# Kernel tuning notes

Measured on AMD Instinct MI355X. Metric: run time of the kernel, lower is better.

Reference implementation:

```python
import jax, jax.numpy as jnp
import numpy as np

HIDDEN = 3584
N_HEADS = 28
N_KV_HEADS = 4
HEAD_DIM = 128
ROPE_BASE = 10000.0
SCALE = HEAD_DIM ** -0.5
T = 2048


def setup_inputs() -> dict:
    key = jax.random.key(0)
    ks = jax.random.split(key, 8)
    s = HIDDEN ** -0.5
    return {
        "positions": jnp.arange(T, dtype=jnp.int64),
        "hidden_states": jax.random.normal(ks[0], (T, HIDDEN), dtype=jnp.float32),
        "wq": jax.random.normal(ks[1], (N_HEADS * HEAD_DIM, HIDDEN), dtype=jnp.float32) * s,
        "bq": jax.random.normal(ks[2], (N_HEADS * HEAD_DIM,), dtype=jnp.float32) * 0.02,
        "wk": jax.random.normal(ks[3], (N_KV_HEADS * HEAD_DIM, HIDDEN), dtype=jnp.float32) * s,
        "bk": jax.random.normal(ks[4], (N_KV_HEADS * HEAD_DIM,), dtype=jnp.float32) * 0.02,
        "wv": jax.random.normal(ks[5], (N_KV_HEADS * HEAD_DIM, HIDDEN), dtype=jnp.float32) * s,
        "bv": jax.random.normal(ks[6], (N_KV_HEADS * HEAD_DIM,), dtype=jnp.float32) * 0.02,
        "wo": jax.random.normal(ks[7], (HIDDEN, N_HEADS * HEAD_DIM), dtype=jnp.float32) * s,
    }


def _rope(x, positions):
    # x: [T, H, D], neox-style rotary over full head_dim
    half = HEAD_DIM // 2
    inv_freq = 1.0 / (ROPE_BASE ** (jnp.arange(half, dtype=jnp.float32) * (2.0 / HEAD_DIM)))
    angles = positions.astype(jnp.float32)[:, None] * inv_freq  # [T, half]
    cos = jnp.cos(angles)[:, None, :]  # [T, 1, half]
    sin = jnp.sin(angles)[:, None, :]
    x1, x2 = x[..., :half], x[..., half:]
    return jnp.concatenate([x1 * cos - x2 * sin, x2 * cos + x1 * sin], axis=-1)


def reference(positions, hidden_states, wq, bq, wk, bk, wv, bv, wo):
    Tn = hidden_states.shape[0]
    q = (hidden_states @ wq.T + bq).reshape(Tn, N_HEADS, HEAD_DIM)
    k = (hidden_states @ wk.T + bk).reshape(Tn, N_KV_HEADS, HEAD_DIM)
    v = (hidden_states @ wv.T + bv).reshape(Tn, N_KV_HEADS, HEAD_DIM)
    q = _rope(q, positions)
    k = _rope(k, positions)
    # GQA: repeat kv heads
    n_rep = N_HEADS // N_KV_HEADS
    k = jnp.repeat(k, n_rep, axis=1)  # [T, H, D]
    v = jnp.repeat(v, n_rep, axis=1)
    # bidirectional (diffusion_lm) attention, no mask
    scores = jnp.einsum("thd,shd->hts", q, k) * SCALE  # [H, T, T]
    probs = jax.nn.softmax(scores, axis=-1)
    o = jnp.einsum("hts,shd->thd", probs, v).reshape(Tn, N_HEADS * HEAD_DIM)
    return o @ wo.T
```

## Files before the change

kernel.cpp:

```cpp
#include <hip/hip_runtime.h>

typedef short bf16x8 __attribute__((ext_vector_type(8)));
typedef float f32x4 __attribute__((ext_vector_type(4)));

#define DEV __device__ __forceinline__

namespace {

constexpr int TSEQ = 2048;
constexpr int HID = 3584;
constexpr int NHEADS = 28;
constexpr int NKVH = 4;
constexpr int HD = 128;
constexpr int NQ = NHEADS * HD;
constexpr int NKV = NKVH * HD;
constexpr int NQKV = NQ + 2 * NKV;
constexpr int QPW = NQ + NKV;

constexpr size_t OFF_BIAS = 0;
constexpr size_t OFF_HB   = 18432;
constexpr size_t OFF_WQKV = OFF_HB + (size_t)TSEQ * HID * 2;
constexpr size_t OFF_QKV0 = OFF_WQKV + (size_t)NQKV * HID * 2;
constexpr size_t OFF_QP   = 18432;
constexpr size_t OFF_VT   = OFF_QP + (size_t)TSEQ * QPW * 2;
constexpr size_t OFF_ATTN = OFF_VT + (size_t)NKVH * HD * TSEQ * 2;
constexpr size_t OFF_WO   = OFF_ATTN + (size_t)TSEQ * NQ * 2;

DEV unsigned short f2bf(float f) {
  unsigned u = __float_as_uint(f);
  u += 0x7FFFu + ((u >> 16) & 1u);
  return (unsigned short)(u >> 16);
}
DEV float bf2f(unsigned short h) { return __uint_as_float(((unsigned)h) << 16); }

DEV void gld_lds16(const void* g, void* l) {
  __builtin_amdgcn_global_load_lds(
      (__attribute__((address_space(1))) void*)(g),
      (__attribute__((address_space(3))) void*)(l), 16, 0, 0);
}

__global__ void cast_kernel(const float* __restrict__ src, unsigned short* __restrict__ dst, int n4) {
  int i = blockIdx.x * 256 + threadIdx.x;
  if (i >= n4) return;
  float4 v = ((const float4*)src)[i];
  ushort4 o;
  o.x = f2bf(v.x); o.y = f2bf(v.y); o.z = f2bf(v.z); o.w = f2bf(v.w);
  ((ushort4*)dst)[i] = o;
}

__global__ void concat_bias(const float* __restrict__ bq, const float* __restrict__ bk,
                            const float* __restrict__ bv, float* __restrict__ dst) {
  int i = blockIdx.x * 256 + threadIdx.x;
  if (i >= NQKV) return;
  float v = (i < NQ) ? bq[i] : (i < NQ + NKV ? bk[i - NQ] : bv[i - NQ - NKV]);
  dst[i] = v;
}

template <bool HAS_BIAS, bool OUT_BF16>
__global__ __launch_bounds__(256, 3)
void gemm_bt(const unsigned short* __restrict__ A, const unsigned short* __restrict__ W,
             const float* __restrict__ bias, void* __restrict__ Cv, int M, int N, int K) {
  __shared__ unsigned short As[128 * 64];
  __shared__ unsigned short Bs[128 * 64];
  const int tid = threadIdx.x;
  const int lane = tid & 63;
  const int wave = tid >> 6;
  const int l15 = lane & 15;
  const int quad = lane >> 4;
  const int wm = wave & 1, wn = wave >> 1;
  const int m0 = blockIdx.y * 128, n0 = blockIdx.x * 128;

  f32x4 acc[4][4] = {};

  const int rowt = tid >> 3;
  const int csrc = (tid & 7) ^ (rowt & 7);
  const unsigned short* gA = A + (size_t)(m0 + rowt) * K + csrc * 8;
  const unsigned short* gB = W + (size_t)(n0 + rowt) * K + csrc * 8;
  char* ldsA = (char*)As + tid * 16;
  char* ldsB = (char*)Bs + tid * 16;

  for (int k0 = 0; k0 < K; k0 += 64) {
#pragma unroll
    for (int r = 0; r < 4; ++r) {
      gld_lds16(gA + (size_t)(r * 32) * K + k0, ldsA + r * 4096);
      gld_lds16(gB + (size_t)(r * 32) * K + k0, ldsB + r * 4096);
    }
    __syncthreads();
    bf16x8 a[2][4], b[2][4];
#pragma unroll
    for (int kq = 0; kq < 2; ++kq) {
      const int cidx = ((kq * 4 + quad) ^ (l15 & 7)) * 8;
#pragma unroll
      for (int i = 0; i < 4; ++i) {
        a[kq][i] = *(const bf16x8*)&As[(wm * 64 + i * 16 + l15) * 64 + cidx];
        b[kq][i] = *(const bf16x8*)&Bs[(wn * 64 + i * 16 + l15) * 64 + cidx];
      }
    }
#pragma unroll
    for (int kq = 0; kq < 2; ++kq)
#pragma unroll
      for (int i = 0; i < 4; ++i)
#pragma unroll
        for (int j = 0; j < 4; ++j)
          acc[i][j] = __builtin_amdgcn_mfma_f32_16x16x32_bf16(a[kq][i], b[kq][j], acc[i][j], 0, 0, 0);
    __syncthreads();
  }

#pragma unroll
  for (int j = 0; j < 4; ++j) {
    const int col = n0 + wn * 64 + j * 16 + l15;
    float bvv = 0.0f;
    if (HAS_BIAS) bvv = bias[col];
#pragma unroll
    for (int i = 0; i < 4; ++i) {
      const int row = m0 + wm * 64 + i * 16 + quad * 4;
#pragma unroll
      for (int r = 0; r < 4; ++r) {
        float v = acc[i][j][r] + bvv;
        if (OUT_BF16)
          ((unsigned short*)Cv)[(size_t)(row + r) * N + col] = f2bf(v);
        else
          ((float*)Cv)[(size_t)(row + r) * N + col] = v;
      }
    }
  }
}

__global__ void rope_kernel(const unsigned short* __restrict__ QKV0, unsigned short* __restrict__ QP) {
  int idx = blockIdx.x * 256 + threadIdx.x;
  int t = idx >> 8;
  int r8 = idx & 255;
  int c1, p0;
  if (r8 < 224) { p0 = (r8 & 7) * 8; c1 = (r8 >> 3) * 128 + p0; }
  else { int rr = r8 - 224; p0 = (rr & 7) * 8; c1 = NQ + (rr >> 3) * 128 + p0; }
  const unsigned short* rowp = QKV0 + (size_t)t * NQKV;
  bf16x8 v1 = *(const bf16x8*)(rowp + c1);
  bf16x8 v2 = *(const bf16x8*)(rowp + c1 + 64);
  bf16x8 o1, o2;
  float tf = (float)t;
#pragma unroll
  for (int j = 0; j < 8; ++j) {
    float x1 = bf2f((unsigned short)v1[j]);
    float x2 = bf2f((unsigned short)v2[j]);
    float inv = exp2f(-(float)(p0 + j) * 0.20762050593045998f);
    float sf, cf;
    __sincosf(tf * inv, &sf, &cf);
    o1[j] = (short)f2bf(x1 * cf - x2 * sf);
    o2[j] = (short)f2bf(x2 * cf + x1 * sf);
  }
  unsigned short* outp = QP + (size_t)t * QPW;
  *(bf16x8*)(outp + c1) = o1;
  *(bf16x8*)(outp + c1 + 64) = o2;
}

__global__ __launch_bounds__(256)
void transpose_v(const unsigned short* __restrict__ QKV0, unsigned short* __restrict__ VT) {
  __shared__ unsigned short tl[64][65];
  const int tid = threadIdx.x;
  const int t0 = blockIdx.x * 64;
  const int c0 = blockIdx.y * 64;
#pragma unroll
  for (int i = 0; i < 4; ++i) {
    int t = i * 16 + (tid >> 4);
    int c = (tid & 15) * 4;
    const unsigned short* g = QKV0 + (size_t)(t0 + t) * NQKV + (NQ + NKV) + c0 + c;
    ushort4 v = *(const ushort4*)g;
    tl[t][c] = v.x; tl[t][c + 1] = v.y; tl[t][c + 2] = v.z; tl[t][c + 3] = v.w;
  }
  __syncthreads();
  const int t_l = tid & 63;
  const int dq = tid >> 6;
#pragma unroll
  for (int j = 0; j < 16; ++j) {
    int d = dq * 16 + j;
    int gc = c0 + d;
    int hkv = gc >> 7;
    int dd = gc & 127;
    VT[(size_t)hkv * (HD * TSEQ) + (size_t)dd * TSEQ + t0 + t_l] = tl[t_l][d];
  }
}

__global__ __launch_bounds__(256, 2)
void attn_kernel(const unsigned short* __restrict__ QP, const unsigned short* __restrict__ VT,
                 unsigned short* __restrict__ O) {
  __shared__ unsigned short lds[32768];
  const int tid = threadIdx.x;
  const int lane = tid & 63;
  const int wv = tid >> 6;
  const int l15 = lane & 15;
  const int quad = lane >> 4;
  const int h = blockIdx.y;
  const int hk = h / 7;
  const int q0 = blockIdx.x * 128;
  const int e8 = (tid & 3) * 8;

#pragma unroll
  for (int i = 0; i < 8; ++i) {
    int kk = i >> 1;
    int q = (i & 1) * 64 + (tid >> 2);
    gld_lds16(QP + (size_t)(q0 + q) * QPW + h * HD + kk * 32 + e8,
              (char*)lds + tid * 16 + i * 4096);
  }
  __syncthreads();
  bf16x8 qf[2][4];
#pragma unroll
  for (int qs = 0; qs < 2; ++qs)
#pragma unroll
    for (int kk = 0; kk < 4; ++kk)
      qf[qs][kk] = *(const bf16x8*)&lds[(kk * 128 + wv * 32 + qs * 16 + l15) * 32 + quad * 8];
  __syncthreads();

  const unsigned short* gK[4];
  const unsigned short* gV[4];
#pragma unroll
  for (int i = 0; i < 4; ++i) {
    gK[i] = QP + (size_t)(tid >> 2) * QPW + NQ + hk * HD + i * 32 + e8;
    int d = (i & 1) * 64 + (tid >> 2);
    gV[i] = VT + (size_t)hk * (HD * TSEQ) + (size_t)d * TSEQ + (i >> 1) * 32 + e8;
  }
#pragma unroll
  for (int i = 0; i < 4; ++i) {
    gld_lds16(gK[i], (char*)lds + tid * 16 + i * 4096);
    gld_lds16(gV[i], (char*)lds + 16384 + tid * 16 + i * 4096);
    gK[i] += (size_t)64 * QPW;
    gV[i] += 64;
  }

  float l_sum[2] = {0.f, 0.f};
  f32x4 o_acc[2][8] = {};
  const float C2 = (float)(0.08838834764831845 * 1.4426950408889634);

  for (int it = 0; it < 32; ++it) {
    __syncthreads();
    if (it < 31) {
      char* nb = (char*)lds + (((it + 1) & 1) << 15);
#pragma unroll
      for (int i = 0; i < 4; ++i) {
        gld_lds16(gK[i], nb + tid * 16 + i * 4096);
        gld_lds16(gV[i], nb + 16384 + tid * 16 + i * 4096);
        gK[i] += (size_t)64 * QPW;
        gV[i] += 64;
      }
    }
    const unsigned short* Kb = lds + ((it & 1) << 14);
    const unsigned short* Vb = Kb + 8192;

    f32x4 s_acc[2][4] = {};
#pragma unroll
    for (int st = 0; st < 4; ++st)
#pragma unroll
      for (int kk = 0; kk < 4; ++kk) {
        bf16x8 kf = *(const bf16x8*)&Kb[(kk * 64 + st * 16 + l15) * 32 + quad * 8];
        s_acc[0][st] = __builtin_amdgcn_mfma_f32_16x16x32_bf16(kf, qf[0][kk], s_acc[0][st], 0, 0, 0);
        s_acc[1][st] = __builtin_amdgcn_mfma_f32_16x16x32_bf16(kf, qf[1][kk], s_acc[1][st], 0, 0, 0);
      }

    unsigned pk[2][4][2];
#pragma unroll
    for (int qs = 0; qs < 2; ++qs) {
      float rs = 0.f;
#pragma unroll
      for (int st = 0; st < 4; ++st) {
        float pp[4];
#pragma unroll
        for (int r = 0; r < 4; ++r) {
          pp[r] = exp2f(s_acc[qs][st][r] * C2);
          rs += pp[r];
        }
        pk[qs][st][0] = __builtin_amdgcn_perm(__float_as_uint(pp[1]) + 0x8000u,
                                              __float_as_uint(pp[0]) + 0x8000u, 0x07060302u);
        pk[qs][st][1] = __builtin_amdgcn_perm(__float_as_uint(pp[3]) + 0x8000u,
                                              __float_as_uint(pp[2]) + 0x8000u, 0x07060302u);
      }
      l_sum[qs] += rs;
    }

    const int sA = ((quad & 1) << 5) + l15;
    const int sB = sA + 16;
    const int hi = quad >> 1;
#pragma unroll
    for (int kk32 = 0; kk32 < 2; ++kk32) {
      union { unsigned u[4]; bf16x8 v; } ap[2];
#pragma unroll
      for (int qs = 0; qs < 2; ++qs) {
        unsigned a0 = __shfl((int)pk[qs][2 * kk32][0], sA);
        unsigned b0 = __shfl((int)pk[qs][2 * kk32 + 1][0], sA);
        unsigned a1 = __shfl((int)pk[qs][2 * kk32][1], sA);
        unsigned b1 = __shfl((int)pk[qs][2 * kk32 + 1][1], sA);
        unsigned a2 = __shfl((int)pk[qs][2 * kk32][0], sB);
        unsigned b2 = __shfl((int)pk[qs][2 * kk32 + 1][0], sB);
        unsigned a3 = __shfl((int)pk[qs][2 * kk32][1], sB);
        unsigned b3 = __shfl((int)pk[qs][2 * kk32 + 1][1], sB);
        ap[qs].u[0] = hi ? b0 : a0;
        ap[qs].u[1] = hi ? b1 : a1;
        ap[qs].u[2] = hi ? b2 : a2;
        ap[qs].u[3] = hi ? b3 : a3;
      }
#pragma unroll
      for (int n = 0; n < 8; ++n) {
        bf16x8 vf = *(const bf16x8*)&Vb[(kk32 * 128 + n * 16 + l15) * 32 + quad * 8];
        o_acc[0][n] = __builtin_amdgcn_mfma_f32_16x16x32_bf16(ap[0].v, vf, o_acc[0][n], 0, 0, 0);
        o_acc[1][n] = __builtin_amdgcn_mfma_f32_16x16x32_bf16(ap[1].v, vf, o_acc[1][n], 0, 0, 0);
      }
    }
  }

#pragma unroll
  for (int qs = 0; qs < 2; ++qs) {
    float lt = l_sum[qs];
    lt += __shfl_xor(lt, 16);
    lt += __shfl_xor(lt, 32);
    float linv[4];
#pragma unroll
    for (int r = 0; r < 4; ++r) linv[r] = 1.0f / __shfl(lt, quad * 4 + r);
#pragma unroll
    for (int n = 0; n < 8; ++n)
#pragma unroll
      for (int r = 0; r < 4; ++r) {
        int row = q0 + wv * 32 + qs * 16 + quad * 4 + r;
        O[(size_t)row * NQ + h * HD + n * 16 + l15] = f2bf(o_acc[qs][n][r] * linv[r]);
      }
  }
}

}

extern "C" void kernel_launch(void* const* d_in, const int* in_sizes, int n_in,
                              void* d_out, int out_size, void* d_ws, size_t ws_size,
                              hipStream_t stream) {
  (void)in_sizes; (void)n_in; (void)out_size; (void)ws_size;
  const float* hidden = (const float*)d_in[1];
  const float* wq = (const float*)d_in[2];
  const float* bq = (const float*)d_in[3];
  const float* wk = (const float*)d_in[4];
  const float* bk = (const float*)d_in[5];
  const float* wv = (const float*)d_in[6];
  const float* bv = (const float*)d_in[7];
  const float* wo = (const float*)d_in[8];

  char* ws = (char*)d_ws;
  float* bias_all       = (float*)(ws + OFF_BIAS);
  unsigned short* Hb    = (unsigned short*)(ws + OFF_HB);
  unsigned short* Wqkv  = (unsigned short*)(ws + OFF_WQKV);
  unsigned short* QKV0  = (unsigned short*)(ws + OFF_QKV0);
  unsigned short* QP    = (unsigned short*)(ws + OFF_QP);
  unsigned short* VTb   = (unsigned short*)(ws + OFF_VT);
  unsigned short* AttnB = (unsigned short*)(ws + OFF_ATTN);
  unsigned short* Wob   = (unsigned short*)(ws + OFF_WO);

  cast_kernel<<<7168, 256, 0, stream>>>(hidden, Hb, TSEQ * HID / 4);
  cast_kernel<<<12544, 256, 0, stream>>>(wq, Wqkv, NQ * HID / 4);
  cast_kernel<<<1792, 256, 0, stream>>>(wk, Wqkv + (size_t)NQ * HID, NKV * HID / 4);
  cast_kernel<<<1792, 256, 0, stream>>>(wv, Wqkv + (size_t)(NQ + NKV) * HID, NKV * HID / 4);
  concat_bias<<<18, 256, 0, stream>>>(bq, bk, bv, bias_all);

  gemm_bt<true, true><<<dim3(NQKV / 128, TSEQ / 128), 256, 0, stream>>>(
      Hb, Wqkv, bias_all, (void*)QKV0, TSEQ, NQKV, HID);

  rope_kernel<<<2048, 256, 0, stream>>>(QKV0, QP);
  transpose_v<<<dim3(TSEQ / 64, NKV / 64), 256, 0, stream>>>(QKV0, VTb);

  cast_kernel<<<12544, 256, 0, stream>>>(wo, Wob, HID * NQ / 4);

  attn_kernel<<<dim3(TSEQ / 128, NHEADS), 256, 0, stream>>>(QP, VTb, AttnB);

  gemm_bt<false, false><<<dim3(NQ / 128, TSEQ / 128), 256, 0, stream>>>(
      AttnB, Wob, nullptr, d_out, TSEQ, HID, NQ);
}
```

Measured before the change: 443.6 us.

## Merge prep launches, fuse rope with V transpose, and cut attention LDS footprint

Folds the four cast kernels and the bias concat into one prep kernel, and merges rope and the V transpose into a single launch. The wo cast now runs as extra blocks of the attention launch. Attention switches to a single V buffer loaded each iteration with an extra barrier, so LDS drops from 64KB to 48KB and launch bounds rise to 3 blocks per SM. The goal is fewer launches and higher occupancy, paid for by V loads that are no longer prefetched a tile ahead and by the extra synchronization.

New measurement: 424.6 us. 4.3% less time.

```diff
diff --git a/kernel.cpp b/kernel.cpp
--- a/kernel.cpp
+++ b/kernel.cpp
@@ -39,21 +39,35 @@
       (__attribute__((address_space(3))) void*)(l), 16, 0, 0);
 }
 
-__global__ void cast_kernel(const float* __restrict__ src, unsigned short* __restrict__ dst, int n4) {
-  int i = blockIdx.x * 256 + threadIdx.x;
-  if (i >= n4) return;
-  float4 v = ((const float4*)src)[i];
+DEV ushort4 cvt4(float4 v) {
   ushort4 o;
   o.x = f2bf(v.x); o.y = f2bf(v.y); o.z = f2bf(v.z); o.w = f2bf(v.w);
-  ((ushort4*)dst)[i] = o;
-}
-
-__global__ void concat_bias(const float* __restrict__ bq, const float* __restrict__ bk,
-                            const float* __restrict__ bv, float* __restrict__ dst) {
-  int i = blockIdx.x * 256 + threadIdx.x;
-  if (i >= NQKV) return;
-  float v = (i < NQ) ? bq[i] : (i < NQ + NKV ? bk[i - NQ] : bv[i - NQ - NKV]);
-  dst[i] = v;
+  return o;
+}
+
+__global__ void prep_kernel(const float* __restrict__ hidden,
+                            const float* __restrict__ wq, const float* __restrict__ wk,
+                            const float* __restrict__ wv,
+                            const float* __restrict__ bq, const float* __restrict__ bk,
+                            const float* __restrict__ bv,
+                            unsigned short* __restrict__ Hb, unsigned short* __restrict__ Wqkv,
+                            float* __restrict__ bias) {
+  int bx = blockIdx.x;
+  if (bx < 7168) {
+    int i = bx * 256 + threadIdx.x;
+    ((ushort4*)Hb)[i] = cvt4(((const float4*)hidden)[i]);
+  } else if (bx < 23296) {
+    int i = (bx - 7168) * 256 + threadIdx.x;
+    const float4* src; int c;
+    if (i < 3211264) { src = (const float4*)wq; c = i; }
+    else if (i < 3670016) { src = (const float4*)wk; c = i - 3211264; }
+    else { src = (const float4*)wv; c = i - 3670016; }
+    ((ushort4*)Wqkv)[i] = cvt4(src[c]);
+  } else {
+    int i = (bx - 23296) * 256 + threadIdx.x;
+    float v = (i < NQ) ? bq[i] : (i < NQ + NKV ? bk[i - NQ] : bv[i - NQ - NKV]);
+    bias[i] = v;
+  }
 }
 
 template <bool HAS_BIAS, bool OUT_BF16>
@@ -126,72 +140,79 @@
   }
 }
 
-__global__ void rope_kernel(const unsigned short* __restrict__ QKV0, unsigned short* __restrict__ QP) {
-  int idx = blockIdx.x * 256 + threadIdx.x;
-  int t = idx >> 8;
-  int r8 = idx & 255;
-  int c1, p0;
-  if (r8 < 224) { p0 = (r8 & 7) * 8; c1 = (r8 >> 3) * 128 + p0; }
-  else { int rr = r8 - 224; p0 = (rr & 7) * 8; c1 = NQ + (rr >> 3) * 128 + p0; }
-  const unsigned short* rowp = QKV0 + (size_t)t * NQKV;
-  bf16x8 v1 = *(const bf16x8*)(rowp + c1);
-  bf16x8 v2 = *(const bf16x8*)(rowp + c1 + 64);
-  bf16x8 o1, o2;
-  float tf = (float)t;
-#pragma unroll
-  for (int j = 0; j < 8; ++j) {
-    float x1 = bf2f((unsigned short)v1[j]);
-    float x2 = bf2f((unsigned short)v2[j]);
-    float inv = exp2f(-(float)(p0 + j) * 0.20762050593045998f);
-    float sf, cf;
-    __sincosf(tf * inv, &sf, &cf);
-    o1[j] = (short)f2bf(x1 * cf - x2 * sf);
-    o2[j] = (short)f2bf(x2 * cf + x1 * sf);
-  }
-  unsigned short* outp = QP + (size_t)t * QPW;
-  *(bf16x8*)(outp + c1) = o1;
-  *(bf16x8*)(outp + c1 + 64) = o2;
-}
-
 __global__ __launch_bounds__(256)
-void transpose_v(const unsigned short* __restrict__ QKV0, unsigned short* __restrict__ VT) {
+void rt_kernel(const unsigned short* __restrict__ QKV0, unsigned short* __restrict__ QP,
+               unsigned short* __restrict__ VT) {
   __shared__ unsigned short tl[64][65];
   const int tid = threadIdx.x;
-  const int t0 = blockIdx.x * 64;
-  const int c0 = blockIdx.y * 64;
-#pragma unroll
-  for (int i = 0; i < 4; ++i) {
-    int t = i * 16 + (tid >> 4);
-    int c = (tid & 15) * 4;
-    const unsigned short* g = QKV0 + (size_t)(t0 + t) * NQKV + (NQ + NKV) + c0 + c;
-    ushort4 v = *(const ushort4*)g;
-    tl[t][c] = v.x; tl[t][c + 1] = v.y; tl[t][c + 2] = v.z; tl[t][c + 3] = v.w;
-  }
-  __syncthreads();
-  const int t_l = tid & 63;
-  const int dq = tid >> 6;
-#pragma unroll
-  for (int j = 0; j < 16; ++j) {
-    int d = dq * 16 + j;
-    int gc = c0 + d;
-    int hkv = gc >> 7;
-    int dd = gc & 127;
-    VT[(size_t)hkv * (HD * TSEQ) + (size_t)dd * TSEQ + t0 + t_l] = tl[t_l][d];
-  }
-}
-
-__global__ __launch_bounds__(256, 2)
+  if (blockIdx.x < 2048) {
+    int t = blockIdx.x;
+    int r8 = tid;
+    int c1, p0;
+    if (r8 < 224) { p0 = (r8 & 7) * 8; c1 = (r8 >> 3) * 128 + p0; }
+    else { int rr = r8 - 224; p0 = (rr & 7) * 8; c1 = NQ + (rr >> 3) * 128 + p0; }
+    const unsigned short* rowp = QKV0 + (size_t)t * NQKV;
+    bf16x8 v1 = *(const bf16x8*)(rowp + c1);
+    bf16x8 v2 = *(const bf16x8*)(rowp + c1 + 64);
+    bf16x8 o1, o2;
+    float tf = (float)t;
+#pragma unroll
+    for (int j = 0; j < 8; ++j) {
+      float x1 = bf2f((unsigned short)v1[j]);
+      float x2 = bf2f((unsigned short)v2[j]);
+      float inv = exp2f(-(float)(p0 + j) * 0.20762050593045998f);
+      float sf, cf;
+      __sincosf(tf * inv, &sf, &cf);
+      o1[j] = (short)f2bf(x1 * cf - x2 * sf);
+      o2[j] = (short)f2bf(x2 * cf + x1 * sf);
+    }
+    unsigned short* outp = QP + (size_t)t * QPW;
+    *(bf16x8*)(outp + c1) = o1;
+    *(bf16x8*)(outp + c1 + 64) = o2;
+  } else {
+    int tb = blockIdx.x - 2048;
+    const int t0 = (tb & 31) * 64;
+    const int c0 = (tb >> 5) * 64;
+#pragma unroll
+    for (int i = 0; i < 4; ++i) {
+      int t = i * 16 + (tid >> 4);
+      int c = (tid & 15) * 4;
+      const unsigned short* g = QKV0 + (size_t)(t0 + t) * NQKV + (NQ + NKV) + c0 + c;
+      ushort4 v = *(const ushort4*)g;
+      tl[t][c] = v.x; tl[t][c + 1] = v.y; tl[t][c + 2] = v.z; tl[t][c + 3] = v.w;
+    }
+    __syncthreads();
+    const int t_l = tid & 63;
+    const int dq = tid >> 6;
+#pragma unroll
+    for (int j = 0; j < 16; ++j) {
+      int d = dq * 16 + j;
+      int gc = c0 + d;
+      int hkv = gc >> 7;
+      int dd = gc & 127;
+      VT[(size_t)hkv * (HD * TSEQ) + (size_t)dd * TSEQ + t0 + t_l] = tl[t_l][d];
+    }
+  }
+}
+
+__global__ __launch_bounds__(256, 3)
 void attn_kernel(const unsigned short* __restrict__ QP, const unsigned short* __restrict__ VT,
-                 unsigned short* __restrict__ O) {
-  __shared__ unsigned short lds[32768];
+                 unsigned short* __restrict__ O,
+                 const float* __restrict__ wo, unsigned short* __restrict__ Wob) {
+  if (blockIdx.x >= 448) {
+    int i = (blockIdx.x - 448) * 256 + threadIdx.x;
+    ((ushort4*)Wob)[i] = cvt4(((const float4*)wo)[i]);
+    return;
+  }
+  __shared__ unsigned short lds[24576];
   const int tid = threadIdx.x;
   const int lane = tid & 63;
   const int wv = tid >> 6;
   const int l15 = lane & 15;
   const int quad = lane >> 4;
-  const int h = blockIdx.y;
+  const int h = blockIdx.x >> 4;
   const int hk = h / 7;
-  const int q0 = blockIdx.x * 128;
+  const int q0 = (blockIdx.x & 15) * 128;
   const int e8 = (tid & 3) * 8;
 
 #pragma unroll
@@ -221,9 +242,7 @@
 #pragma unroll
   for (int i = 0; i < 4; ++i) {
     gld_lds16(gK[i], (char*)lds + tid * 16 + i * 4096);
-    gld_lds16(gV[i], (char*)lds + 16384 + tid * 16 + i * 4096);
     gK[i] += (size_t)64 * QPW;
-    gV[i] += 64;
   }
 
   float l_sum[2] = {0.f, 0.f};
@@ -232,18 +251,20 @@
 
   for (int it = 0; it < 32; ++it) {
     __syncthreads();
-    if (it < 31) {
-      char* nb = (char*)lds + (((it + 1) & 1) << 15);
-#pragma unroll
-      for (int i = 0; i < 4; ++i) {
-        gld_lds16(gK[i], nb + tid * 16 + i * 4096);
-        gld_lds16(gV[i], nb + 16384 + tid * 16 + i * 4096);
-        gK[i] += (size_t)64 * QPW;
-        gV[i] += 64;
-      }
-    }
-    const unsigned short* Kb = lds + ((it & 1) << 14);
-    const unsigned short* Vb = Kb + 8192;
+    {
+      char* vb = (char*)lds + 32768;
+#pragma unroll
+      for (int i = 0; i < 4; ++i) { gld_lds16(gV[i], vb + tid * 16 + i * 4096); gV[i] += 64; }
+      if (it < 31) {
+        char* kb = (char*)lds + (((it + 1) & 1) << 14);
+#pragma unroll
+        for (int i = 0; i < 4; ++i) {
+          gld_lds16(gK[i], kb + tid * 16 + i * 4096);
+          gK[i] += (size_t)64 * QPW;
+        }
+      }
+    }
+    const unsigned short* Kb = lds + ((it & 1) << 13);
 
     f32x4 s_acc[2][4] = {};
 #pragma unroll
@@ -274,6 +295,9 @@
       }
       l_sum[qs] += rs;
     }
+
+    __syncthreads();
+    const unsigned short* Vb = lds + 16384;
 
     const int sA = ((quad & 1) << 5) + l15;
     const int sB = sA + 16;
@@ -348,21 +372,14 @@
   unsigned short* AttnB = (unsigned short*)(ws + OFF_ATTN);
   unsigned short* Wob   = (unsigned short*)(ws + OFF_WO);
 
-  cast_kernel<<<7168, 256, 0, stream>>>(hidden, Hb, TSEQ * HID / 4);
-  cast_kernel<<<12544, 256, 0, stream>>>(wq, Wqkv, NQ * HID / 4);
-  cast_kernel<<<1792, 256, 0, stream>>>(wk, Wqkv + (size_t)NQ * HID, NKV * HID / 4);
-  cast_kernel<<<1792, 256, 0, stream>>>(wv, Wqkv + (size_t)(NQ + NKV) * HID, NKV * HID / 4);
-  concat_bias<<<18, 256, 0, stream>>>(bq, bk, bv, bias_all);
+  prep_kernel<<<23314, 256, 0, stream>>>(hidden, wq, wk, wv, bq, bk, bv, Hb, Wqkv, bias_all);
 
   gemm_bt<true, true><<<dim3(NQKV / 128, TSEQ / 128), 256, 0, stream>>>(
       Hb, Wqkv, bias_all, (void*)QKV0, TSEQ, NQKV, HID);
 
-  rope_kernel<<<2048, 256, 0, stream>>>(QKV0, QP);
-  transpose_v<<<dim3(TSEQ / 64, NKV / 64), 256, 0, stream>>>(QKV0, VTb);
-
-  cast_kernel<<<12544, 256, 0, stream>>>(wo, Wob, HID * NQ / 4);
-
-  attn_kernel<<<dim3(TSEQ / 128, NHEADS), 256, 0, stream>>>(QP, VTb, AttnB);
+  rt_kernel<<<2304, 256, 0, stream>>>(QKV0, QP, VTb);
+
+  attn_kernel<<<448 + 12544, 256, 0, stream>>>(QP, VTb, AttnB, wo, Wob);
 
   gemm_bt<false, false><<<dim3(NQ / 128, TSEQ / 128), 256, 0, stream>>>(
       AttnB, Wob, nullptr, d_out, TSEQ, HID, NQ);
```
